# Kernel tuning notes

Measured on AMD Instinct MI355X. Metric: run time of the kernel, lower is better.

Reference implementation:

```python
import jax, jax.numpy as jnp
import numpy as np

B, N, H = 131072, 16, 64  # batch, num_static, hidden_layer_size
EPS = 1e-5

def _ln(y, gamma, beta):
    mu = y.mean(-1, keepdims=True)
    var = y.var(-1, keepdims=True)
    return gamma * (y - mu) / jnp.sqrt(var + EPS) + beta

def setup_inputs() -> dict:
    key = jax.random.key(0)
    ks = jax.random.split(key, 12)
    def p(k, shape, fan_in):
        return (jax.random.normal(k, shape, jnp.float32) / np.float32(np.sqrt(fan_in)))
    F = N * H
    return dict(
        embedding=jax.random.normal(ks[0], (B, N, H), jnp.float32),
        # flattened GRN (input F=N*H, hidden H, output N): selection weights
        W1f=p(ks[1], (F, H), F), b1f=jnp.zeros((H,), jnp.float32),
        W2f=p(ks[2], (H, H), H), b2f=jnp.zeros((H,), jnp.float32),
        Wvf=p(ks[3], (H, N), H), bvf=jnp.zeros((N,), jnp.float32),
        Wgf=p(ks[4], (H, N), H), bgf=jnp.zeros((N,), jnp.float32),
        Wsf=p(ks[5], (F, N), F), bsf=jnp.zeros((N,), jnp.float32),
        gf=jnp.ones((N,), jnp.float32), betaf=jnp.zeros((N,), jnp.float32),
        # per-variable GRNs (input H, hidden H, output H, identity skip), stacked over N
        W1v=p(ks[6], (N, H, H), H), b1v=jnp.zeros((N, H), jnp.float32),
        W2v=p(ks[7], (N, H, H), H), b2v=jnp.zeros((N, H), jnp.float32),
        Wvv=p(ks[8], (N, H, H), H), bvv=jnp.zeros((N, H), jnp.float32),
        Wgv=p(ks[9], (N, H, H), H), bgv=jnp.zeros((N, H), jnp.float32),
        gv=jnp.ones((N, H), jnp.float32), betav=jnp.zeros((N, H), jnp.float32),
    )

def reference(embedding, W1f, b1f, W2f, b2f, Wvf, bvf, Wgf, bgf, Wsf, bsf, gf, betaf,
              W1v, b1v, W2v, b2v, Wvv, bvv, Wgv, bgv, gv, betav):
    Bsz = embedding.shape[0]
    flat = embedding.reshape(Bsz, -1)  # [B, N*H]
    # flattened GRN -> variable-selection logits [B, N]
    h = jax.nn.elu(flat @ W1f + b1f)
    h = h @ W2f + b2f
    glu = (h @ Wvf + bvf) * jax.nn.sigmoid(h @ Wgf + bgf)
    skip = flat @ Wsf + bsf  # skip projection since output dim N != input dim
    logits = _ln(skip + glu, gf, betaf)
    sparse_weights = jax.nn.softmax(logits, axis=1)[:, :, None]  # [B, N, 1]
    # num_static per-variable GRNs, batched across the variable axis: [B, N, H]
    hv = jax.nn.elu(jnp.einsum('bnh,nhk->bnk', embedding, W1v) + b1v)
    hv = jnp.einsum('bnh,nhk->bnk', hv, W2v) + b2v
    gluv = (jnp.einsum('bnh,nhk->bnk', hv, Wvv) + bvv) * jax.nn.sigmoid(
        jnp.einsum('bnh,nhk->bnk', hv, Wgv) + bgv)
    transformed = _ln(embedding + gluv, gv, betav)  # identity skip (output_size=None)
    static_vec = (transformed * sparse_weights).sum(axis=1)  # [B, H]
    return (static_vec, sparse_weights)
```

## Files before the change

kernel.cpp:

```cpp
#include <hip/hip_runtime.h>
#include <stdint.h>
#include <stddef.h>

typedef unsigned short ushort;
typedef __attribute__((ext_vector_type(8))) short short8;
typedef __attribute__((ext_vector_type(8))) unsigned short ushort8;
typedef __attribute__((ext_vector_type(4))) unsigned int u32x4;
typedef __attribute__((ext_vector_type(4))) float f32x4;

#define MFMA16(A, B, C) __builtin_amdgcn_mfma_f32_16x16x32_bf16(A, B, C, 0, 0, 0)

static constexpr int NV = 16;
static constexpr int FF = 1024;
static constexpr int BATCH = 131072;

static constexpr size_t WS_W1T   = 8;
static constexpr size_t WS_WST   = 65544;
static constexpr size_t WS_W2T   = 81928;
static constexpr size_t WS_WVT   = 86024;
static constexpr size_t WS_WGT   = 87048;
static constexpr size_t WS_W1VT  = 88072;
static constexpr size_t WS_W2VT  = 153608;
static constexpr size_t WS_WVVT  = 219144;
static constexpr size_t WS_WGVT  = 284680;
static constexpr size_t WS_PAR   = 350216;
static constexpr size_t WS_PAR2  = 356576;
static constexpr int P_B1F = 0, P_B2F = 64, P_BVF = 128, P_BGF = 144, P_BSF = 160,
                     P_GF = 176, P_BETAF = 192, P_B1V = 208, P_B2V = 1232,
                     P_BVV = 2256, P_BGV = 3280, P_GV = 4304, P_BETAV = 5328;

__device__ __forceinline__ float bf2f(ushort b) {
  return __builtin_bit_cast(float, (unsigned)b << 16);
}
__device__ __forceinline__ ushort f2bf(float x) {
  unsigned u = __builtin_bit_cast(unsigned, x);
  return (ushort)((u + 0x7fffu + ((u >> 16) & 1u)) >> 16);
}
__device__ __forceinline__ unsigned cvtpk(float lo, float hi) {
  unsigned r;
  asm("v_cvt_pk_bf16_f32 %0, %1, %2" : "=v"(r) : "v"(lo), "v"(hi));
  return r;
}
__device__ __forceinline__ short8 ld8(const ushort* p) {
  return __builtin_bit_cast(short8, *(const ushort8*)p);
}
__device__ __forceinline__ ushort8 cvt8(const f32x4 a, const f32x4 b) {
  u32x4 w;
  w[0] = cvtpk(a[0], a[1]); w[1] = cvtpk(a[2], a[3]);
  w[2] = cvtpk(b[0], b[1]); w[3] = cvtpk(b[2], b[3]);
  return __builtin_bit_cast(ushort8, w);
}

__device__ __forceinline__ int swzb(int row, int bo) { return bo ^ ((row & 7) << 4); }

typedef const __attribute__((address_space(1))) void gvoid;
typedef __attribute__((address_space(3))) void lvoid;
__device__ __forceinline__ void glds16(const void* g, void* l) {
  __builtin_amdgcn_global_load_lds((gvoid*)g, (lvoid*)l, 16, 0, 0);
}

__global__ void set_flag(const unsigned* __restrict__ gf, int* __restrict__ flag) {
  if (threadIdx.x == 0 && blockIdx.x == 0)
    *flag = (gf[0] == 0x3F800000u) ? 1 : 0;
}

__global__ void repack_all(const void* s0, const void* s1, const void* s2,
                           const void* s3, const void* s4, const void* s5,
                           const void* s6, const void* s7, const void* s8,
                           ushort* __restrict__ ws, const int* __restrict__ flagp) {
  const int flag = *flagp;
  const void* srcs[9] = {s0, s1, s2, s3, s4, s5, s6, s7, s8};
  const int RR[9]  = {1024, 1024, 64, 64, 64, 64, 64, 64, 64};
  const int CC[9]  = {64, 16, 64, 16, 16, 64, 64, 64, 64};
  const int CNT[9] = {65536, 16384, 4096, 1024, 1024, 65536, 65536, 65536, 65536};
  const size_t DOF[9] = {WS_W1T, WS_WST, WS_W2T, WS_WVT, WS_WGT,
                         WS_W1VT, WS_W2VT, WS_WVVT, WS_WGVT};
  const int total = 350208;
  for (int idx = blockIdx.x * blockDim.x + threadIdx.x; idx < total;
       idx += gridDim.x * blockDim.x) {
    int seg = 0, off = idx;
    while (off >= CNT[seg]) { off -= CNT[seg]; ++seg; }
    const int R = RR[seg], C = CC[seg];
    const int b = off / (R * C);
    const int rem = off - b * R * C;
    const int r = rem / C;
    const int c = rem - r * C;
    const ushort v = flag ? f2bf(((const float*)srcs[seg])[off])
                          : ((const ushort*)srcs[seg])[off];
    ws[DOF[seg] + (size_t)(b * C + c) * R + r] = v;
  }
}

__global__ void pack_params(const void* s0, const void* s1, const void* s2,
                            const void* s3, const void* s4, const void* s5,
                            const void* s6, const void* s7, const void* s8,
                            const void* s9, const void* s10, const void* s11,
                            const void* s12, ushort* __restrict__ dst,
                            const int* __restrict__ flagp) {
  const int flag = *flagp;
  const void* srcs[13] = {s0, s1, s2, s3, s4, s5, s6, s7, s8, s9, s10, s11, s12};
  const int sizes[13] = {64, 64, 16, 16, 16, 16, 16, 1024, 1024, 1024, 1024, 1024, 1024};
  const int offs[13]  = {P_B1F, P_B2F, P_BVF, P_BGF, P_BSF, P_GF, P_BETAF,
                         P_B1V, P_B2V, P_BVV, P_BGV, P_GV, P_BETAV};
  const int seg = blockIdx.x;
  if (seg < 13) {
    const void* s = srcs[seg];
    for (int i = threadIdx.x; i < sizes[seg]; i += blockDim.x) {
      ushort v = flag ? f2bf(((const float*)s)[i]) : ((const ushort*)s)[i];
      dst[offs[seg] + i] = v;
    }
  } else {
    const void* vsrc[6] = {s7, s8, s9, s10, s11, s12};
    ushort* p2 = dst + (WS_PAR2 - WS_PAR);
    for (int i = threadIdx.x; i < 16 * 64 * 8; i += blockDim.x) {
      const int c = i >> 3;
      const int p = i & 7;
      ushort v = 0;
      if (p < 6) v = flag ? f2bf(((const float*)vsrc[p])[c]) : ((const ushort*)vsrc[p])[c];
      p2[i] = v;
    }
  }
}

template<int FLAG>
__launch_bounds__(256, 2)
__global__ void k1_weights(const void* __restrict__ embv,
                           const ushort* __restrict__ ws,
                           const int* __restrict__ flagp,
                           void* __restrict__ outbase)
{
  if (*flagp != FLAG) return;
  __shared__ __align__(16) ushort lds[128 * 128 + 80 * 128];
  const int tid = threadIdx.x;
  const int wid = tid >> 6;
  const int lane = tid & 63;
  const int g = lane >> 4;
  const int l16 = lane & 15;
  const int r0 = blockIdx.x * 128;

  const ushort* w1t = ws + WS_W1T;
  const ushort* wst = ws + WS_WST;
  const ushort* w2t = ws + WS_W2T;
  const ushort* wvt = ws + WS_WVT;
  const ushort* wgt = ws + WS_WGT;
  const ushort* par = ws + WS_PAR;
  const float* embf = (const float*)embv;
  const ushort* embb = (const ushort*)embv;

  f32x4 hacc[2][4];
  f32x4 sacc[2];
  #pragma unroll
  for (int mt = 0; mt < 2; ++mt) {
    #pragma unroll
    for (int jt = 0; jt < 4; ++jt) hacc[mt][jt] = {0.f, 0.f, 0.f, 0.f};
    sacc[mt] = {0.f, 0.f, 0.f, 0.f};
  }

  f32x4 pr[8][2];
  auto issueE = [&](int kc) {
    const int k0 = kc * 128;
    #pragma unroll
    for (int i = 0; i < 8; ++i) {
      const int row = (wid * 8 + i) * 4 + (lane >> 4);
      const int eo = (lane & 15) * 8;
      const float* gp = &embf[(size_t)(r0 + row) * FF + k0 + eo];
      pr[i][0] = *(const f32x4*)gp;
      pr[i][1] = *(const f32x4*)(gp + 4);
    }
  };

  if constexpr (FLAG) issueE(0);

  for (int kc = 0; kc < 8; ++kc) {
    const int k0 = kc * 128;
    #pragma unroll
    for (int i = 0; i < 5; ++i) {
      const int rb = (wid * 5 + i) * 4;
      const int row = rb + (lane >> 4);
      const int bo = (lane & 15) * 16;
      const ushort* srcb = (row < 64) ? (w1t + (size_t)row * FF)
                                      : (wst + (size_t)(row - 64) * FF);
      const char* gp = (const char*)(srcb + k0) + swzb(row, bo);
      glds16(gp, (void*)&lds[16384 + rb * 128]);
    }
    if constexpr (FLAG) {
      #pragma unroll
      for (int i = 0; i < 8; ++i) {
        const int row = (wid * 8 + i) * 4 + (lane >> 4);
        const int eo = (lane & 15) * 8;
        *(ushort8*)&lds[row * 128 + (swzb(row, eo * 2) >> 1)] = cvt8(pr[i][0], pr[i][1]);
      }
      if (kc < 7) issueE(kc + 1);
    } else {
      #pragma unroll
      for (int i = 0; i < 8; ++i) {
        const int rb = (wid * 8 + i) * 4;
        const int row = rb + (lane >> 4);
        const int bo = (lane & 15) * 16;
        const char* gp = (const char*)embb + ((size_t)(r0 + row) * FF + k0) * 2 + swzb(row, bo);
        glds16(gp, (void*)&lds[rb * 128]);
      }
    }
    __syncthreads();
    #pragma unroll
    for (int ks = 0; ks < 4; ++ks) {
      short8 a[2];
      #pragma unroll
      for (int mt = 0; mt < 2; ++mt) {
        const int row = wid * 32 + mt * 16 + l16;
        a[mt] = ld8(&lds[row * 128 + (swzb(row, ks * 64 + g * 16) >> 1)]);
      }
      #pragma unroll
      for (int jt = 0; jt < 4; ++jt) {
        const int wr = jt * 16 + l16;
        const short8 b = ld8(&lds[16384 + wr * 128 + (swzb(wr, ks * 64 + g * 16) >> 1)]);
        #pragma unroll
        for (int mt = 0; mt < 2; ++mt) hacc[mt][jt] = MFMA16(a[mt], b, hacc[mt][jt]);
      }
      {
        const int wr = 64 + l16;
        const short8 b = ld8(&lds[16384 + wr * 128 + (swzb(wr, ks * 64 + g * 16) >> 1)]);
        #pragma unroll
        for (int mt = 0; mt < 2; ++mt) sacc[mt] = MFMA16(a[mt], b, sacc[mt]);
      }
    }
    __syncthreads();
  }

  ushort* scr = &lds[wid * 2048];

  {
    float bb1[4];
    #pragma unroll
    for (int jt = 0; jt < 4; ++jt) bb1[jt] = bf2f(par[P_B1F + jt * 16 + l16]);
    #pragma unroll
    for (int mt = 0; mt < 2; ++mt)
      #pragma unroll
      for (int jt = 0; jt < 4; ++jt)
        #pragma unroll
        for (int r = 0; r < 4; ++r) {
          float x = hacc[mt][jt][r] + bb1[jt];
          x = (x > 0.f) ? x : (__expf(x) - 1.f);
          const int row = mt * 16 + g * 4 + r;
          scr[row * 64 + (swzb(row, (jt * 16 + l16) * 2) >> 1)] = (ushort)cvtpk(x, x);
        }
  }

  f32x4 h2a[2][4];
  #pragma unroll
  for (int mt = 0; mt < 2; ++mt)
    #pragma unroll
    for (int jt = 0; jt < 4; ++jt) h2a[mt][jt] = {0.f, 0.f, 0.f, 0.f};
  #pragma unroll
  for (int ks = 0; ks < 2; ++ks) {
    short8 a[2];
    #pragma unroll
    for (int mt = 0; mt < 2; ++mt) {
      const int row = mt * 16 + l16;
      a[mt] = ld8(&scr[row * 64 + (swzb(row, ks * 64 + g * 16) >> 1)]);
    }
    #pragma unroll
    for (int jt = 0; jt < 4; ++jt) {
      const short8 b = ld8(&w2t[(size_t)(jt * 16 + l16) * 64 + ks * 32 + g * 8]);
      #pragma unroll
      for (int mt = 0; mt < 2; ++mt) h2a[mt][jt] = MFMA16(a[mt], b, h2a[mt][jt]);
    }
  }
  {
    float bb2[4];
    #pragma unroll
    for (int jt = 0; jt < 4; ++jt) bb2[jt] = bf2f(par[P_B2F + jt * 16 + l16]);
    #pragma unroll
    for (int mt = 0; mt < 2; ++mt)
      #pragma unroll
      for (int jt = 0; jt < 4; ++jt)
        #pragma unroll
        for (int r = 0; r < 4; ++r) {
          const int row = mt * 16 + g * 4 + r;
          const float x = h2a[mt][jt][r] + bb2[jt];
          scr[row * 64 + (swzb(row, (jt * 16 + l16) * 2) >> 1)] = (ushort)cvtpk(x, x);
        }
  }

  f32x4 vacc[2], gacc[2];
  #pragma unroll
  for (int mt = 0; mt < 2; ++mt) { vacc[mt] = {0.f,0.f,0.f,0.f}; gacc[mt] = {0.f,0.f,0.f,0.f}; }
  #pragma unroll
  for (int ks = 0; ks < 2; ++ks) {
    short8 a[2];
    #pragma unroll
    for (int mt = 0; mt < 2; ++mt) {
      const int row = mt * 16 + l16;
      a[mt] = ld8(&scr[row * 64 + (swzb(row, ks * 64 + g * 16) >> 1)]);
    }
    const short8 bv = ld8(&wvt[(size_t)l16 * 64 + ks * 32 + g * 8]);
    const short8 bg = ld8(&wgt[(size_t)l16 * 64 + ks * 32 + g * 8]);
    #pragma unroll
    for (int mt = 0; mt < 2; ++mt) {
      vacc[mt] = MFMA16(a[mt], bv, vacc[mt]);
      gacc[mt] = MFMA16(a[mt], bg, gacc[mt]);
    }
  }

  const float cbv = bf2f(par[P_BVF + l16]), cbg = bf2f(par[P_BGF + l16]);
  const float cbs = bf2f(par[P_BSF + l16]);
  const float cgf = bf2f(par[P_GF + l16]), cbf = bf2f(par[P_BETAF + l16]);
  #pragma unroll
  for (int mt = 0; mt < 2; ++mt)
    #pragma unroll
    for (int r = 0; r < 4; ++r) {
      const float v  = vacc[mt][r] + cbv;
      const float gg = gacc[mt][r] + cbg;
      const float glu = v / (1.f + __expf(-gg));
      const float pre = sacc[mt][r] + cbs + glu;
      float s1 = pre, s2 = pre * pre;
      #pragma unroll
      for (int d = 1; d < 16; d <<= 1) { s1 += __shfl_xor(s1, d); s2 += __shfl_xor(s2, d); }
      const float mu = s1 * (1.f / 16.f);
      const float var = s2 * (1.f / 16.f) - mu * mu;
      const float rstd = rsqrtf(var + 1e-5f);
      const float ln = cgf * (pre - mu) * rstd + cbf;
      float mx = ln;
      #pragma unroll
      for (int d = 1; d < 16; d <<= 1) mx = fmaxf(mx, __shfl_xor(mx, d));
      const float e = __expf(ln - mx);
      float se = e;
      #pragma unroll
      for (int d = 1; d < 16; d <<= 1) se += __shfl_xor(se, d);
      const float wv = e / se;
      const size_t idx = (size_t)(r0 + wid * 32 + mt * 16 + g * 4 + r) * 16 + l16;
      if constexpr (FLAG) ((float*)outbase + (size_t)BATCH * 64)[idx] = wv;
      else                ((ushort*)outbase + (size_t)BATCH * 64)[idx] = f2bf(wv);
    }
}

template<int FLAG>
__launch_bounds__(256, 2)
__global__ void k3_combine(const void* __restrict__ embv,
                           const ushort* __restrict__ ws,
                           const int* __restrict__ flagp,
                           void* __restrict__ outbase)
{
  if (*flagp != FLAG) return;
  __shared__ __align__(16) ushort lds[36864];
  const int tid = threadIdx.x;
  const int wid = tid >> 6;
  const int lane = tid & 63;
  const int g = lane >> 4;
  const int l16 = lane & 15;
  const int r0 = blockIdx.x * 128;

  const ushort* w1vt = ws + WS_W1VT;
  const ushort* w2vt = ws + WS_W2VT;
  const ushort* wvvt = ws + WS_WVVT;
  const ushort* wgvt = ws + WS_WGVT;
  const ushort* p2   = ws + WS_PAR2;
  const float* embf = (const float*)embv;
  const ushort* embb = (const ushort*)embv;
  float* swlf = (float*)&lds[24576];
  ushort* scr = &lds[28672 + wid * 2048];

  f32x4 pr[4][2];
  auto issueE = [&](int n) {
    #pragma unroll
    for (int i = 0; i < 4; ++i) {
      const int row = (wid * 4 + i) * 8 + (lane >> 3);
      const int eo = (lane & 7) * 8;
      const float* gp = &embf[(size_t)(r0 + row) * FF + n * 64 + eo];
      pr[i][0] = *(const f32x4*)gp;
      pr[i][1] = *(const f32x4*)(gp + 4);
    }
  };
  auto writeE = [&]() {
    #pragma unroll
    for (int i = 0; i < 4; ++i) {
      const int row = (wid * 4 + i) * 8 + (lane >> 3);
      const int eo = (lane & 7) * 8;
      *(ushort8*)&lds[row * 64 + (swzb(row, eo * 2) >> 1)] = cvt8(pr[i][0], pr[i][1]);
    }
  };
  auto gldsE = [&](int n) {
    #pragma unroll
    for (int i = 0; i < 4; ++i) {
      const int rb = (wid * 4 + i) * 8;
      const int row = rb + (lane >> 3);
      const int bo = (lane & 7) * 16;
      const char* gp = (const char*)embb + ((size_t)(r0 + row) * FF + n * 64) * 2 + swzb(row, bo);
      glds16(gp, (void*)&lds[rb * 64]);
    }
  };
  auto stageW = [&](int n) {
    #pragma unroll
    for (int i = 0; i < 8; ++i) {
      const int rb = (wid * 8 + i) * 8;
      const int wr = rb + (lane >> 3);
      const int mat = wr >> 6;
      const int rin = wr & 63;
      const ushort* base = (mat == 0) ? w1vt : (mat == 1) ? w2vt : (mat == 2) ? wvvt : wgvt;
      const int bo = (lane & 7) * 16;
      const char* gp = (const char*)(base + ((size_t)n * 64 + rin) * 64) + swzb(rin, bo);
      glds16(gp, (void*)&lds[8192 + rb * 64]);
    }
  };

  if constexpr (FLAG) {
    const float* swg = (const float*)outbase + (size_t)BATCH * 64;
    #pragma unroll
    for (int j = 0; j < 2; ++j) {
      const int rr = (wid * 2 + j) * 16 + (lane >> 2);
      const float* gp = &swg[(size_t)(r0 + rr) * 16 + (lane & 3) * 4];
      glds16(gp, (void*)((char*)swlf + (wid * 2 + j) * 1024));
    }
  } else {
    const ushort* swg = (const ushort*)outbase + (size_t)BATCH * 64;
    const int row = wid * 32 + (lane >> 1);
    const char* gp = (const char*)swg + ((size_t)(r0 + row) * 16 + (lane & 1) * 8) * 2;
    glds16(gp, (void*)&lds[24576 + wid * 512]);
  }
  stageW(0);
  if constexpr (FLAG) { issueE(0); writeE(); } else gldsE(0);
  __syncthreads();

  f32x4 st[2][4];
  #pragma unroll
  for (int mt = 0; mt < 2; ++mt)
    #pragma unroll
    for (int jt = 0; jt < 4; ++jt) st[mt][jt] = {0.f, 0.f, 0.f, 0.f};

  for (int n = 0; n < NV; ++n) {
    if constexpr (FLAG) { if (n < 15) issueE(n + 1); }

    float bb1[4], bb2[4], bbv[4], bbg[4], cg[4], cb[4];
    #pragma unroll
    for (int jt = 0; jt < 4; ++jt) {
      const ushort8 pv = *(const ushort8*)&p2[(((size_t)(n * 4 + jt) * 16) + l16) * 8];
      bb1[jt] = bf2f(pv[0]); bb2[jt] = bf2f(pv[1]);
      bbv[jt] = bf2f(pv[2]); bbg[jt] = bf2f(pv[3]);
      cg[jt]  = bf2f(pv[4]); cb[jt]  = bf2f(pv[5]);
    }

    f32x4 acc[2][4];
    #pragma unroll
    for (int mt = 0; mt < 2; ++mt)
      #pragma unroll
      for (int jt = 0; jt < 4; ++jt) acc[mt][jt] = {0.f, 0.f, 0.f, 0.f};
    #pragma unroll
    for (int ks = 0; ks < 2; ++ks) {
      short8 a[2];
      #pragma unroll
      for (int mt = 0; mt < 2; ++mt) {
        const int row = wid * 32 + mt * 16 + l16;
        a[mt] = ld8(&lds[row * 64 + (swzb(row, ks * 64 + g * 16) >> 1)]);
      }
      #pragma unroll
      for (int jt = 0; jt < 4; ++jt) {
        const int wr = jt * 16 + l16;
        const short8 b = ld8(&lds[8192 + wr * 64 + (swzb(wr, ks * 64 + g * 16) >> 1)]);
        #pragma unroll
        for (int mt = 0; mt < 2; ++mt) acc[mt][jt] = MFMA16(a[mt], b, acc[mt][jt]);
      }
    }
    #pragma unroll
    for (int mt = 0; mt < 2; ++mt)
      #pragma unroll
      for (int jt = 0; jt < 4; ++jt)
        #pragma unroll
        for (int r = 0; r < 4; ++r) {
          float x = acc[mt][jt][r] + bb1[jt];
          x = (x > 0.f) ? x : (__expf(x) - 1.f);
          const int row = mt * 16 + g * 4 + r;
          scr[row * 64 + (swzb(row, (jt * 16 + l16) * 2) >> 1)] = (ushort)cvtpk(x, x);
        }

    #pragma unroll
    for (int mt = 0; mt < 2; ++mt)
      #pragma unroll
      for (int jt = 0; jt < 4; ++jt) acc[mt][jt] = {0.f, 0.f, 0.f, 0.f};
    #pragma unroll
    for (int ks = 0; ks < 2; ++ks) {
      short8 a[2];
      #pragma unroll
      for (int mt = 0; mt < 2; ++mt) {
        const int row = mt * 16 + l16;
        a[mt] = ld8(&scr[row * 64 + (swzb(row, ks * 64 + g * 16) >> 1)]);
      }
      #pragma unroll
      for (int jt = 0; jt < 4; ++jt) {
        const int wr = 64 + jt * 16 + l16;
        const short8 b = ld8(&lds[8192 + wr * 64 + (swzb(wr, ks * 64 + g * 16) >> 1)]);
        #pragma unroll
        for (int mt = 0; mt < 2; ++mt) acc[mt][jt] = MFMA16(a[mt], b, acc[mt][jt]);
      }
    }
    #pragma unroll
    for (int mt = 0; mt < 2; ++mt)
      #pragma unroll
      for (int jt = 0; jt < 4; ++jt)
        #pragma unroll
        for (int r = 0; r < 4; ++r) {
          const int row = mt * 16 + g * 4 + r;
          const float x = acc[mt][jt][r] + bb2[jt];
          scr[row * 64 + (swzb(row, (jt * 16 + l16) * 2) >> 1)] = (ushort)cvtpk(x, x);
        }

    f32x4 av[2][4], ag[2][4];
    #pragma unroll
    for (int mt = 0; mt < 2; ++mt)
      #pragma unroll
      for (int jt = 0; jt < 4; ++jt) { av[mt][jt] = {0.f,0.f,0.f,0.f}; ag[mt][jt] = {0.f,0.f,0.f,0.f}; }
    #pragma unroll
    for (int ks = 0; ks < 2; ++ks) {
      short8 a[2];
      #pragma unroll
      for (int mt = 0; mt < 2; ++mt) {
        const int row = mt * 16 + l16;
        a[mt] = ld8(&scr[row * 64 + (swzb(row, ks * 64 + g * 16) >> 1)]);
      }
      #pragma unroll
      for (int jt = 0; jt < 4; ++jt) {
        const int wrv = 128 + jt * 16 + l16;
        const int wrg = 192 + jt * 16 + l16;
        const short8 bv = ld8(&lds[8192 + wrv * 64 + (swzb(wrv, ks * 64 + g * 16) >> 1)]);
        const short8 bg = ld8(&lds[8192 + wrg * 64 + (swzb(wrg, ks * 64 + g * 16) >> 1)]);
        #pragma unroll
        for (int mt = 0; mt < 2; ++mt) {
          av[mt][jt] = MFMA16(a[mt], bv, av[mt][jt]);
          ag[mt][jt] = MFMA16(a[mt], bg, ag[mt][jt]);
        }
      }
    }

    #pragma unroll
    for (int mt = 0; mt < 2; ++mt)
      #pragma unroll
      for (int r = 0; r < 4; ++r) {
        const int lrow = wid * 32 + mt * 16 + g * 4 + r;
        float wv;
        if constexpr (FLAG) wv = swlf[lrow * 16 + n];
        else                wv = bf2f(lds[24576 + lrow * 16 + n]);
        float x[4];
        float s1 = 0.f, s2 = 0.f;
        #pragma unroll
        for (int jt = 0; jt < 4; ++jt) {
          const float vv = av[mt][jt][r] + bbv[jt];
          const float gg = ag[mt][jt][r] + bbg[jt];
          const float glu = vv / (1.f + __expf(-gg));
          const float e = bf2f(lds[lrow * 64 + (swzb(lrow, (jt * 16 + l16) * 2) >> 1)]);
          const float y = e + glu;
          x[jt] = y; s1 += y; s2 += y * y;
        }
        #pragma unroll
        for (int d = 1; d < 16; d <<= 1) { s1 += __shfl_xor(s1, d); s2 += __shfl_xor(s2, d); }
        const float mu = s1 * (1.f / 64.f);
        const float varr = s2 * (1.f / 64.f) - mu * mu;
        const float rstd = rsqrtf(varr + 1e-5f);
        #pragma unroll
        for (int jt = 0; jt < 4; ++jt) {
          const float t = cg[jt] * (x[jt] - mu) * rstd + cb[jt];
          st[mt][jt][r] += wv * t;
        }
      }

    __syncthreads();
    if (n < 15) {
      stageW(n + 1);
      if constexpr (FLAG) writeE();
      else                gldsE(n + 1);
    }
    __syncthreads();
  }

  #pragma unroll
  for (int mt = 0; mt < 2; ++mt)
    #pragma unroll
    for (int jt = 0; jt < 4; ++jt)
      #pragma unroll
      for (int r = 0; r < 4; ++r) {
        const size_t idx = (size_t)(r0 + wid * 32 + mt * 16 + g * 4 + r) * 64 + jt * 16 + l16;
        if constexpr (FLAG) ((float*)outbase)[idx] = st[mt][jt][r];
        else                ((ushort*)outbase)[idx] = f2bf(st[mt][jt][r]);
      }
}

extern "C" void kernel_launch(void* const* d_in, const int* in_sizes, int n_in,
                              void* d_out, int out_size, void* d_ws, size_t ws_size,
                              hipStream_t stream) {
  ushort* ws = (ushort*)d_ws;
  int* flag = (int*)d_ws;

  set_flag<<<1, 64, 0, stream>>>((const unsigned*)d_in[11], flag);

  repack_all<<<512, 256, 0, stream>>>(d_in[1], d_in[9], d_in[3], d_in[5], d_in[7],
                                      d_in[13], d_in[15], d_in[17], d_in[19], ws, flag);

  pack_params<<<14, 256, 0, stream>>>(d_in[2], d_in[4], d_in[6], d_in[8], d_in[10],
                                      d_in[11], d_in[12], d_in[14], d_in[16],
                                      d_in[18], d_in[20], d_in[21], d_in[22],
                                      ws + WS_PAR, flag);

  k1_weights<1><<<BATCH / 128, 256, 0, stream>>>(d_in[0], ws, flag, d_out);
  k1_weights<0><<<BATCH / 128, 256, 0, stream>>>(d_in[0], ws, flag, d_out);
  k3_combine<1><<<BATCH / 128, 256, 0, stream>>>(d_in[0], ws, flag, d_out);
  k3_combine<0><<<BATCH / 128, 256, 0, stream>>>(d_in[0], ws, flag, d_out);
}
```

Measured before the change: 448.9 us.

## Shrink LDS footprint in combine kernel to raise occupancy and reorder staging

Cuts the combine kernel's shared memory from 36864 to 24576 ushorts by placing the per-wave scratch over the embedding tile region and reading selection weights straight from global memory into registers. The embedding values are copied into registers before the first GEMM so that region can be reused, and the GLU/LayerNorm accumulation is fused per output tile. Launch bounds rise to 3 blocks per SM, and the next-stage weight/embedding loads are issued right after the first barrier so they overlap the LayerNorm reduction. The risk is more register pressure under the tighter launch bound, plus uncoalesced scalar global loads for the weights.

New measurement: 1.087 ms. 2.42x slower.

```diff
diff --git a/kernel.cpp b/kernel.cpp
--- a/kernel.cpp
+++ b/kernel.cpp
@@ -335,14 +335,14 @@
 }
 
 template<int FLAG>
-__launch_bounds__(256, 2)
+__launch_bounds__(256, 3)
 __global__ void k3_combine(const void* __restrict__ embv,
                            const ushort* __restrict__ ws,
                            const int* __restrict__ flagp,
                            void* __restrict__ outbase)
 {
   if (*flagp != FLAG) return;
-  __shared__ __align__(16) ushort lds[36864];
+  __shared__ __align__(16) ushort lds[24576];
   const int tid = threadIdx.x;
   const int wid = tid >> 6;
   const int lane = tid & 63;
@@ -357,18 +357,19 @@
   const ushort* p2   = ws + WS_PAR2;
   const float* embf = (const float*)embv;
   const ushort* embb = (const ushort*)embv;
-  float* swlf = (float*)&lds[24576];
-  ushort* scr = &lds[28672 + wid * 2048];
-
-  f32x4 pr[4][2];
+  const float* swgf = (const float*)outbase + (size_t)BATCH * 64;
+  const ushort* swgb = (const ushort*)outbase + (size_t)BATCH * 64;
+  ushort* scr = &lds[wid * 2048];
+
+  f32x4 prE[4][2];
   auto issueE = [&](int n) {
     #pragma unroll
     for (int i = 0; i < 4; ++i) {
       const int row = (wid * 4 + i) * 8 + (lane >> 3);
       const int eo = (lane & 7) * 8;
       const float* gp = &embf[(size_t)(r0 + row) * FF + n * 64 + eo];
-      pr[i][0] = *(const f32x4*)gp;
-      pr[i][1] = *(const f32x4*)(gp + 4);
+      prE[i][0] = *(const f32x4*)gp;
+      prE[i][1] = *(const f32x4*)(gp + 4);
     }
   };
   auto writeE = [&]() {
@@ -376,7 +377,7 @@
     for (int i = 0; i < 4; ++i) {
       const int row = (wid * 4 + i) * 8 + (lane >> 3);
       const int eo = (lane & 7) * 8;
-      *(ushort8*)&lds[row * 64 + (swzb(row, eo * 2) >> 1)] = cvt8(pr[i][0], pr[i][1]);
+      *(ushort8*)&lds[row * 64 + (swzb(row, eo * 2) >> 1)] = cvt8(prE[i][0], prE[i][1]);
     }
   };
   auto gldsE = [&](int n) {
@@ -403,33 +404,18 @@
     }
   };
 
-  if constexpr (FLAG) {
-    const float* swg = (const float*)outbase + (size_t)BATCH * 64;
-    #pragma unroll
-    for (int j = 0; j < 2; ++j) {
-      const int rr = (wid * 2 + j) * 16 + (lane >> 2);
-      const float* gp = &swg[(size_t)(r0 + rr) * 16 + (lane & 3) * 4];
-      glds16(gp, (void*)((char*)swlf + (wid * 2 + j) * 1024));
-    }
-  } else {
-    const ushort* swg = (const ushort*)outbase + (size_t)BATCH * 64;
-    const int row = wid * 32 + (lane >> 1);
-    const char* gp = (const char*)swg + ((size_t)(r0 + row) * 16 + (lane & 1) * 8) * 2;
-    glds16(gp, (void*)&lds[24576 + wid * 512]);
-  }
   stageW(0);
   if constexpr (FLAG) { issueE(0); writeE(); } else gldsE(0);
+
+  f32x4 st[2][4];
+  #pragma unroll
+  for (int mt = 0; mt < 2; ++mt)
+    #pragma unroll
+    for (int jt = 0; jt < 4; ++jt) st[mt][jt] = {0.f, 0.f, 0.f, 0.f};
+
   __syncthreads();
 
-  f32x4 st[2][4];
-  #pragma unroll
-  for (int mt = 0; mt < 2; ++mt)
-    #pragma unroll
-    for (int jt = 0; jt < 4; ++jt) st[mt][jt] = {0.f, 0.f, 0.f, 0.f};
-
   for (int n = 0; n < NV; ++n) {
-    if constexpr (FLAG) { if (n < 15) issueE(n + 1); }
-
     float bb1[4], bb2[4], bbv[4], bbg[4], cg[4], cb[4];
     #pragma unroll
     for (int jt = 0; jt < 4; ++jt) {
@@ -439,6 +425,27 @@
       cg[jt]  = bf2f(pv[4]); cb[jt]  = bf2f(pv[5]);
     }
 
+    float wvp[2][4];
+    #pragma unroll
+    for (int mt = 0; mt < 2; ++mt)
+      #pragma unroll
+      for (int r = 0; r < 4; ++r) {
+        const size_t lrow = (size_t)(r0 + wid * 32 + mt * 16 + g * 4 + r);
+        if constexpr (FLAG) wvp[mt][r] = swgf[lrow * 16 + n];
+        else                wvp[mt][r] = bf2f(swgb[lrow * 16 + n]);
+      }
+
+    float er[2][4][4];
+    #pragma unroll
+    for (int mt = 0; mt < 2; ++mt)
+      #pragma unroll
+      for (int jt = 0; jt < 4; ++jt)
+        #pragma unroll
+        for (int r = 0; r < 4; ++r) {
+          const int lrow = wid * 32 + mt * 16 + g * 4 + r;
+          er[mt][jt][r] = bf2f(lds[lrow * 64 + (swzb(lrow, (jt * 16 + l16) * 2) >> 1)]);
+        }
+
     f32x4 acc[2][4];
     #pragma unroll
     for (int mt = 0; mt < 2; ++mt)
@@ -503,70 +510,75 @@
           scr[row * 64 + (swzb(row, (jt * 16 + l16) * 2) >> 1)] = (ushort)cvtpk(x, x);
         }
 
-    f32x4 av[2][4], ag[2][4];
-    #pragma unroll
-    for (int mt = 0; mt < 2; ++mt)
-      #pragma unroll
-      for (int jt = 0; jt < 4; ++jt) { av[mt][jt] = {0.f,0.f,0.f,0.f}; ag[mt][jt] = {0.f,0.f,0.f,0.f}; }
-    #pragma unroll
-    for (int ks = 0; ks < 2; ++ks) {
-      short8 a[2];
+    short8 a2[2][2];
+    #pragma unroll
+    for (int ks = 0; ks < 2; ++ks)
       #pragma unroll
       for (int mt = 0; mt < 2; ++mt) {
         const int row = mt * 16 + l16;
-        a[mt] = ld8(&scr[row * 64 + (swzb(row, ks * 64 + g * 16) >> 1)]);
-      }
-      #pragma unroll
-      for (int jt = 0; jt < 4; ++jt) {
+        a2[ks][mt] = ld8(&scr[row * 64 + (swzb(row, ks * 64 + g * 16) >> 1)]);
+      }
+    f32x4 x[2][4];
+    f32x4 s1v[2], s2v[2];
+    #pragma unroll
+    for (int mt = 0; mt < 2; ++mt) { s1v[mt] = {0.f,0.f,0.f,0.f}; s2v[mt] = {0.f,0.f,0.f,0.f}; }
+    #pragma unroll
+    for (int jt = 0; jt < 4; ++jt) {
+      f32x4 avj[2], agj[2];
+      #pragma unroll
+      for (int mt = 0; mt < 2; ++mt) { avj[mt] = {0.f,0.f,0.f,0.f}; agj[mt] = {0.f,0.f,0.f,0.f}; }
+      #pragma unroll
+      for (int ks = 0; ks < 2; ++ks) {
         const int wrv = 128 + jt * 16 + l16;
         const int wrg = 192 + jt * 16 + l16;
         const short8 bv = ld8(&lds[8192 + wrv * 64 + (swzb(wrv, ks * 64 + g * 16) >> 1)]);
         const short8 bg = ld8(&lds[8192 + wrg * 64 + (swzb(wrg, ks * 64 + g * 16) >> 1)]);
         #pragma unroll
         for (int mt = 0; mt < 2; ++mt) {
-          av[mt][jt] = MFMA16(a[mt], bv, av[mt][jt]);
-          ag[mt][jt] = MFMA16(a[mt], bg, ag[mt][jt]);
-        }
-      }
+          avj[mt] = MFMA16(a2[ks][mt], bv, avj[mt]);
+          agj[mt] = MFMA16(a2[ks][mt], bg, agj[mt]);
+        }
+      }
+      #pragma unroll
+      for (int mt = 0; mt < 2; ++mt)
+        #pragma unroll
+        for (int r = 0; r < 4; ++r) {
+          const float vv = avj[mt][r] + bbv[jt];
+          const float gg = agj[mt][r] + bbg[jt];
+          const float glu = vv / (1.f + __expf(-gg));
+          const float y = er[mt][jt][r] + glu;
+          x[mt][jt][r] = y;
+          s1v[mt][r] += y;
+          s2v[mt][r] += y * y;
+        }
+    }
+
+    __syncthreads();
+    if (n < NV - 1) {
+      stageW(n + 1);
+      if constexpr (FLAG) issueE(n + 1);
+      else                gldsE(n + 1);
     }
 
     #pragma unroll
     for (int mt = 0; mt < 2; ++mt)
       #pragma unroll
       for (int r = 0; r < 4; ++r) {
-        const int lrow = wid * 32 + mt * 16 + g * 4 + r;
-        float wv;
-        if constexpr (FLAG) wv = swlf[lrow * 16 + n];
-        else                wv = bf2f(lds[24576 + lrow * 16 + n]);
-        float x[4];
-        float s1 = 0.f, s2 = 0.f;
-        #pragma unroll
-        for (int jt = 0; jt < 4; ++jt) {
-          const float vv = av[mt][jt][r] + bbv[jt];
-          const float gg = ag[mt][jt][r] + bbg[jt];
-          const float glu = vv / (1.f + __expf(-gg));
-          const float e = bf2f(lds[lrow * 64 + (swzb(lrow, (jt * 16 + l16) * 2) >> 1)]);
-          const float y = e + glu;
-          x[jt] = y; s1 += y; s2 += y * y;
-        }
+        float s1 = s1v[mt][r], s2 = s2v[mt][r];
         #pragma unroll
         for (int d = 1; d < 16; d <<= 1) { s1 += __shfl_xor(s1, d); s2 += __shfl_xor(s2, d); }
+        const float wv = wvp[mt][r];
         const float mu = s1 * (1.f / 64.f);
         const float varr = s2 * (1.f / 64.f) - mu * mu;
         const float rstd = rsqrtf(varr + 1e-5f);
         #pragma unroll
         for (int jt = 0; jt < 4; ++jt) {
-          const float t = cg[jt] * (x[jt] - mu) * rstd + cb[jt];
+          const float t = cg[jt] * (x[mt][jt][r] - mu) * rstd + cb[jt];
           st[mt][jt][r] += wv * t;
         }
       }
 
-    __syncthreads();
-    if (n < 15) {
-      stageW(n + 1);
-      if constexpr (FLAG) writeE();
-      else                gldsE(n + 1);
-    }
+    if constexpr (FLAG) { if (n < NV - 1) writeE(); }
     __syncthreads();
   }
 
```
